# Kernel tuning notes

Hardware: AMD Instinct MI355X
Metric: run time of the kernel (lower is better)

Reference implementation:

```python
import jax, jax.numpy as jnp
import numpy as np

H = 1024

def setup_inputs() -> dict:
    key = jax.random.key(0)
    ks = jax.random.split(key, 9)
    s = 1.0 / np.sqrt(H)
    x = jax.random.normal(ks[0], (4, 2048, H), dtype=jnp.float32)
    Wq = jax.random.uniform(ks[1], (H, H), jnp.float32, -s, s)
    bq = jax.random.uniform(ks[2], (H,), jnp.float32, -s, s)
    Wk = jax.random.uniform(ks[3], (H, H), jnp.float32, -s, s)
    bk = jax.random.uniform(ks[4], (H,), jnp.float32, -s, s)
    Wv = jax.random.uniform(ks[5], (H, H), jnp.float32, -s, s)
    bv = jax.random.uniform(ks[6], (H,), jnp.float32, -s, s)
    Wo = jax.random.uniform(ks[7], (H, H), jnp.float32, -s, s)
    bo = jax.random.uniform(ks[8], (H,), jnp.float32, -s, s)
    return {"x": x, "Wq": Wq, "bq": bq, "Wk": Wk, "bk": bk,
            "Wv": Wv, "bv": bv, "Wo": Wo, "bo": bo}

def reference(x, Wq, bq, Wk, bk, Wv, bv, Wo, bo):
    # Linear uses y = x @ W.T + b (torch convention: W is [out, in])
    q = jnp.einsum('bsd,ed->bse', x, Wq) + bq
    k = jnp.einsum('bsd,ed->bse', x, Wk) + bk
    v = jnp.einsum('bsd,ed->bse', x, Wv) + bv
    scale = q.shape[-1] ** 0.5
    attn = jnp.einsum('bqe,bke->bqk', q, k) / scale  # [B,S,S]
    attn = jax.nn.softmax(attn, axis=-1)
    out = jnp.einsum('bqk,bke->bqe', attn, v)
    return jnp.einsum('bse,oe->bso', out, Wo) + bo
```

## Files before the change

### kernel.cpp

```cpp
#include <hip/hip_runtime.h>

typedef short  short4v __attribute__((ext_vector_type(4)));
typedef short  short8v __attribute__((ext_vector_type(8)));
typedef __bf16 bf16x8  __attribute__((ext_vector_type(8)));
typedef float  f32x4   __attribute__((ext_vector_type(4)));
typedef float  float4v __attribute__((ext_vector_type(4)));

__device__ __forceinline__ short f2bf(float f) {
  unsigned u = __builtin_bit_cast(unsigned, f);
  u += 0x7fffu + ((u >> 16) & 1u);
  return (short)(u >> 16);
}
__device__ __forceinline__ float bf2f(short h) {
  unsigned u = ((unsigned)(unsigned short)h) << 16;
  return __builtin_bit_cast(float, u);
}
__device__ __forceinline__ bf16x8 ld8(const short* p) {
  return __builtin_bit_cast(bf16x8, *reinterpret_cast<const short8v*>(p));
}

__global__ __launch_bounds__(256) void k_cvt(const float* __restrict__ in,
                                             short* __restrict__ out, int n4) {
  int i = blockIdx.x * 256 + threadIdx.x;
  if (i >= n4) return;
  float4v v = *reinterpret_cast<const float4v*>(in + (long)i * 4);
  short4v o;
  o[0] = f2bf(v[0]); o[1] = f2bf(v[1]); o[2] = f2bf(v[2]); o[3] = f2bf(v[3]);
  *reinterpret_cast<short4v*>(out + (long)i * 4) = o;
}

__global__ __launch_bounds__(256) void k_cvtT(const float* __restrict__ i0,
    const float* __restrict__ i1, const float* __restrict__ i2,
    const float* __restrict__ i3, short* __restrict__ o0, short* __restrict__ o1,
    short* __restrict__ o2, short* __restrict__ o3) {
  const int z = blockIdx.z;
  const float* in = z == 0 ? i0 : z == 1 ? i1 : z == 2 ? i2 : i3;
  short* out = z == 0 ? o0 : z == 1 ? o1 : z == 2 ? o2 : o3;
  __shared__ float tile[16][17];
  const int lx = threadIdx.x & 15, ly = threadIdx.x >> 4;
  const int bx = blockIdx.x << 4, by = blockIdx.y << 4;
  float v = in[(long)(by + ly) * 1024 + bx + lx];
  if (z == 3) {
    out[(long)(by + ly) * 1024 + bx + lx] = f2bf(v);
    return;
  }
  tile[ly][lx] = v;
  __syncthreads();
  out[(long)(bx + ly) * 1024 + by + lx] = f2bf(tile[lx][ly]);
}

__global__ __launch_bounds__(256) void k_vecprep(
    const short* __restrict__ wkT, const float* __restrict__ bq,
    const float* __restrict__ Wo, const float* __restrict__ bv,
    float* __restrict__ bvec, float* __restrict__ bvp) {
  const int row = blockIdx.x * 4 + (threadIdx.x >> 6), lane = threadIdx.x & 63;
  float s = 0.f;
  if (blockIdx.z == 0) {
    const short* xr = wkT + (long)row * 1024 + lane * 16;
    short8v a0 = *reinterpret_cast<const short8v*>(xr);
    short8v a1 = *reinterpret_cast<const short8v*>(xr + 8);
#pragma unroll
    for (int j = 0; j < 8; ++j) s += bf2f(a0[j]) * bq[lane * 16 + j];
#pragma unroll
    for (int j = 0; j < 8; ++j) s += bf2f(a1[j]) * bq[lane * 16 + 8 + j];
  } else {
#pragma unroll
    for (int j = 0; j < 16; ++j)
      s += Wo[(long)row * 1024 + j * 64 + lane] * bv[j * 64 + lane];
  }
#pragma unroll
  for (int off = 32; off; off >>= 1) s += __shfl_xor(s, off);
  if (lane == 0) (blockIdx.z == 0 ? bvec : bvp)[row] = s;
}

__global__ __launch_bounds__(256) void k_rowdot(const short* __restrict__ X,
    const float* __restrict__ v, float* __restrict__ o) {
  const int row = blockIdx.x * 4 + (threadIdx.x >> 6), lane = threadIdx.x & 63;
  const short* xr = X + (long)row * 1024 + lane * 16;
  short8v a0 = *reinterpret_cast<const short8v*>(xr);
  short8v a1 = *reinterpret_cast<const short8v*>(xr + 8);
  float s = 0.f;
#pragma unroll
  for (int j = 0; j < 8; ++j) s += bf2f(a0[j]) * v[lane * 16 + j];
#pragma unroll
  for (int j = 0; j < 8; ++j) s += bf2f(a1[j]) * v[lane * 16 + 8 + j];
#pragma unroll
  for (int off = 32; off; off >>= 1) s += __shfl_xor(s, off);
  if (lane == 0) o[row] = s;
}

template <int MODE>
__global__ __launch_bounds__(256, 3) void k_gemm(
    const short* __restrict__ A, const short* __restrict__ B,
    const float* __restrict__ b0p, float* __restrict__ b1p,
    void* __restrict__ C0,
    int K, int lda, int ldb, long sA, long sB, long sC, int ldC) {
  __shared__ __align__(16) short lsA[128 * 64];
  __shared__ __align__(16) short lsB[128 * 64];
  __shared__ float invL[128];
  const int tid = threadIdx.x;
  const int lane = tid & 63, wid = tid >> 6;
  const int wr = wid >> 1, wc = wid & 1;
  const int fr = lane & 15, fq = lane >> 4;
  const int bm = blockIdx.x * 128, bn = blockIdx.y * 128;
  const int bz = blockIdx.z;
  const short* Ab = A + (long)bz * sA;
  const short* Bb = B + (long)bz * sB;

  if constexpr (MODE == 4) {
    if (tid < 128) {
      const float* pr = b1p + ((long)bz * 2048 + bm + tid) * 32;
      float s = 0.f;
#pragma unroll
      for (int j = 0; j < 32; ++j) s += pr[j];
      invL[tid] = 1.0f / s;
    }
  }

  f32x4 acc[4][4] = {};

  for (int kt = 0; kt < K; kt += 64) {
    __syncthreads();
#pragma unroll
    for (int c = 0; c < 4; ++c) {
      const int idx = c * 256 + tid;
      const int row = idx >> 3, colh = (idx & 7) << 3;
      const short* ga = Ab + (long)(bm + row) * lda + kt + colh;
      const short* gb = Bb + (long)(bn + row) * ldb + kt + colh;
      __builtin_amdgcn_global_load_lds(
          (const __attribute__((address_space(1))) void*)ga,
          (__attribute__((address_space(3))) void*)&lsA[idx * 8], 16, 0, 0);
      __builtin_amdgcn_global_load_lds(
          (const __attribute__((address_space(1))) void*)gb,
          (__attribute__((address_space(3))) void*)&lsB[idx * 8], 16, 0, 0);
    }
    __syncthreads();
#pragma unroll
    for (int ks = 0; ks < 64; ks += 32) {
      bf16x8 a[4], b[4];
#pragma unroll
      for (int m = 0; m < 4; ++m)
        a[m] = ld8(&lsA[(wr * 64 + m * 16 + fr) * 64 + ks + fq * 8]);
#pragma unroll
      for (int n = 0; n < 4; ++n)
        b[n] = ld8(&lsB[(wc * 64 + n * 16 + fr) * 64 + ks + fq * 8]);
#pragma unroll
      for (int m = 0; m < 4; ++m)
#pragma unroll
        for (int n = 0; n < 4; ++n)
          acc[m][n] = __builtin_amdgcn_mfma_f32_16x16x32_bf16(a[m], b[n], acc[m][n], 0, 0, 0);
    }
  }

  if constexpr (MODE == 3) {
    constexpr float c = 0.03125f * 1.44269504f;
    short* O = (short*)C0 + (long)bz * sC;
    float wv[4];
#pragma unroll
    for (int n = 0; n < 4; ++n)
      wv[n] = b0p[(long)bz * 2048 + bn + wc * 64 + n * 16 + fr];
#pragma unroll
    for (int m = 0; m < 4; ++m) {
#pragma unroll
      for (int i = 0; i < 4; ++i) {
        const int row = bm + wr * 64 + m * 16 + fq * 4 + i;
        float rs = 0.f;
#pragma unroll
        for (int n = 0; n < 4; ++n) {
          float e = exp2f((acc[m][n][i] + wv[n]) * c);
          O[(long)row * ldC + bn + wc * 64 + n * 16 + fr] = f2bf(e);
          rs += e;
        }
        rs += __shfl_xor(rs, 1); rs += __shfl_xor(rs, 2);
        rs += __shfl_xor(rs, 4); rs += __shfl_xor(rs, 8);
        if (fr == 0)
          b1p[((long)bz * 2048 + row) * 32 + (blockIdx.y << 1) + wc] = rs;
      }
    }
  } else {
#pragma unroll
    for (int n = 0; n < 4; ++n) {
      const int coll = wc * 64 + n * 16 + fr;
#pragma unroll
      for (int m = 0; m < 4; ++m) {
        const int rl0 = wr * 64 + m * 16 + fq * 4;
#pragma unroll
        for (int i = 0; i < 4; ++i) {
          const float vacc = acc[m][n][i];
          const long row = bm + rl0 + i, col = bn + coll;
          if constexpr (MODE == 0) {
            ((short*)C0)[((long)bz * sC) + row * ldC + col] = f2bf(vacc);
          } else if constexpr (MODE == 5) {
            ((short*)C0)[row * ldC + col] = f2bf(vacc + b0p[row]);
          } else {
            float* O = (float*)C0 + (long)bz * sC;
            O[row * ldC + col] = vacc * invL[rl0 + i] + b0p[col];
          }
        }
      }
    }
  }
}

extern "C" void kernel_launch(void* const* d_in, const int* in_sizes, int n_in,
                              void* d_out, int out_size, void* d_ws, size_t ws_size,
                              hipStream_t stream) {
  const float* x  = (const float*)d_in[0];
  const float* Wq = (const float*)d_in[1];
  const float* bq = (const float*)d_in[2];
  const float* Wk = (const float*)d_in[3];
  const float* Wv = (const float*)d_in[5];
  const float* bv = (const float*)d_in[6];
  const float* Wo = (const float*)d_in[7];
  const float* bo = (const float*)d_in[8];

  char* ws = (char*)d_ws;
  short* xb   = (short*)ws; ws += 8192L * 1024 * 2;
  short* wkT  = (short*)ws; ws += 1024L * 1024 * 2;
  short* wob  = (short*)ws; ws += 1024L * 1024 * 2;
  short* wqT  = (short*)ws; ws += 1024L * 1024 * 2;
  short* wvT  = (short*)ws; ws += 1024L * 1024 * 2;
  short* mt   = (short*)ws; ws += 1024L * 1024 * 2;
  short* wv2  = (short*)ws; ws += 1024L * 1024 * 2;
  short* T    = (short*)ws; ws += 8192L * 1024 * 2;
  short* vTp  = (short*)ws; ws += 1024L * 8192 * 2;
  short* Sc   = (short*)ws; ws += 4L * 2048 * 2048 * 2;
  float* psum = (float*)ws; ws += 4L * 2048 * 32 * 4;
  float* w8   = (float*)ws; ws += 8192L * 4;
  float* bvec = (float*)ws; ws += 1024L * 4;
  float* bvp  = (float*)ws; ws += 1024L * 4;

  dim3 b256(256);
  k_cvt<<<8192, b256, 0, stream>>>(x, xb, 2097152);
  k_cvtT<<<dim3(64, 64, 4), b256, 0, stream>>>(
      Wk, Wq, Wv, Wo, wkT, wqT, wvT, wob);
  k_vecprep<<<dim3(256, 1, 2), b256, 0, stream>>>(wkT, bq, Wo, bv, bvec, bvp);
  k_rowdot<<<2048, b256, 0, stream>>>(xb, bvec, w8);

  k_gemm<0><<<dim3(8, 8, 2), b256, 0, stream>>>(
      wkT, wqT, nullptr, nullptr, mt,
      1024, 1024, 1024, 1024L * 1024, 1024L * 1024, 1024L * 1024, 1024);
  k_gemm<0><<<dim3(64, 8, 1), b256, 0, stream>>>(
      xb, mt, nullptr, nullptr, T, 1024, 1024, 1024, 0, 0, 0, 1024);
  k_gemm<5><<<dim3(8, 64, 1), b256, 0, stream>>>(
      wv2, xb, bvp, nullptr, vTp, 1024, 1024, 1024, 0, 0, 0, 8192);
  k_gemm<3><<<dim3(16, 16, 4), b256, 0, stream>>>(
      T, xb, w8, psum, Sc,
      1024, 1024, 1024, 2048L * 1024, 2048L * 1024, 2048L * 2048, 2048);
  k_gemm<4><<<dim3(16, 8, 4), b256, 0, stream>>>(
      Sc, vTp, bo, psum, (float*)d_out,
      2048, 2048, 8192, 2048L * 2048, 2048, 2048L * 1024, 1024);
}
```

Measured before the change: 212.3 us.

## Merge T/V GEMMs and rowdot into one launch; fold softmax scale into weights

```diff
diff --git a/kernel.cpp b/kernel.cpp
--- a/kernel.cpp
+++ b/kernel.cpp
@@ -18,6 +18,8 @@
 __device__ __forceinline__ bf16x8 ld8(const short* p) {
   return __builtin_bit_cast(bf16x8, *reinterpret_cast<const short8v*>(p));
 }
+
+__constant__ const float kExpScale = 0.04508422f;
 
 __global__ __launch_bounds__(256) void k_cvt(const float* __restrict__ in,
                                              short* __restrict__ out, int n4) {
@@ -29,24 +31,48 @@
   *reinterpret_cast<short4v*>(out + (long)i * 4) = o;
 }
 
-__global__ __launch_bounds__(256) void k_cvtT(const float* __restrict__ i0,
+__global__ __launch_bounds__(256) void k_wprep(const float* __restrict__ i0,
     const float* __restrict__ i1, const float* __restrict__ i2,
     const float* __restrict__ i3, short* __restrict__ o0, short* __restrict__ o1,
     short* __restrict__ o2, short* __restrict__ o3) {
   const int z = blockIdx.z;
   const float* in = z == 0 ? i0 : z == 1 ? i1 : z == 2 ? i2 : i3;
   short* out = z == 0 ? o0 : z == 1 ? o1 : z == 2 ? o2 : o3;
-  __shared__ float tile[16][17];
-  const int lx = threadIdx.x & 15, ly = threadIdx.x >> 4;
-  const int bx = blockIdx.x << 4, by = blockIdx.y << 4;
-  float v = in[(long)(by + ly) * 1024 + bx + lx];
+  const float sc = (z == 1) ? kExpScale : 1.0f;
+  const int tid = threadIdx.x;
+  const int c0 = blockIdx.x << 6;
+  const int r0 = blockIdx.y << 7;
   if (z == 3) {
-    out[(long)(by + ly) * 1024 + bx + lx] = f2bf(v);
+#pragma unroll
+    for (int j = 0; j < 8; ++j) {
+      int idx = j * 256 + tid;
+      int r = idx >> 4, c4 = (idx & 15) << 2;
+      float4v v = *reinterpret_cast<const float4v*>(in + (long)(r0 + r) * 1024 + c0 + c4);
+      short4v o;
+      o[0] = f2bf(v[0]); o[1] = f2bf(v[1]); o[2] = f2bf(v[2]); o[3] = f2bf(v[3]);
+      *reinterpret_cast<short4v*>(out + (long)(r0 + r) * 1024 + c0 + c4) = o;
+    }
     return;
   }
-  tile[ly][lx] = v;
+  __shared__ float tile[128][65];
+#pragma unroll
+  for (int j = 0; j < 8; ++j) {
+    int idx = j * 256 + tid;
+    int r = idx >> 4, c4 = (idx & 15) << 2;
+    float4v v = *reinterpret_cast<const float4v*>(in + (long)(r0 + r) * 1024 + c0 + c4);
+    tile[r][c4 + 0] = v[0] * sc; tile[r][c4 + 1] = v[1] * sc;
+    tile[r][c4 + 2] = v[2] * sc; tile[r][c4 + 3] = v[3] * sc;
+  }
   __syncthreads();
-  out[(long)(bx + ly) * 1024 + by + lx] = f2bf(tile[lx][ly]);
+#pragma unroll
+  for (int j = 0; j < 8; ++j) {
+    int idx = j * 256 + tid;
+    int rO = idx >> 5, g4 = (idx & 31) << 2;
+    short4v o;
+    o[0] = f2bf(tile[g4 + 0][rO]); o[1] = f2bf(tile[g4 + 1][rO]);
+    o[2] = f2bf(tile[g4 + 2][rO]); o[3] = f2bf(tile[g4 + 3][rO]);
+    *reinterpret_cast<short4v*>(out + (long)(c0 + rO) * 1024 + r0 + g4) = o;
+  }
 }
 
 __global__ __launch_bounds__(256) void k_vecprep(
@@ -63,6 +89,7 @@
     for (int j = 0; j < 8; ++j) s += bf2f(a0[j]) * bq[lane * 16 + j];
 #pragma unroll
     for (int j = 0; j < 8; ++j) s += bf2f(a1[j]) * bq[lane * 16 + 8 + j];
+    s *= kExpScale;
   } else {
 #pragma unroll
     for (int j = 0; j < 16; ++j)
@@ -73,52 +100,15 @@
   if (lane == 0) (blockIdx.z == 0 ? bvec : bvp)[row] = s;
 }
 
-__global__ __launch_bounds__(256) void k_rowdot(const short* __restrict__ X,
-    const float* __restrict__ v, float* __restrict__ o) {
-  const int row = blockIdx.x * 4 + (threadIdx.x >> 6), lane = threadIdx.x & 63;
-  const short* xr = X + (long)row * 1024 + lane * 16;
-  short8v a0 = *reinterpret_cast<const short8v*>(xr);
-  short8v a1 = *reinterpret_cast<const short8v*>(xr + 8);
-  float s = 0.f;
-#pragma unroll
-  for (int j = 0; j < 8; ++j) s += bf2f(a0[j]) * v[lane * 16 + j];
-#pragma unroll
-  for (int j = 0; j < 8; ++j) s += bf2f(a1[j]) * v[lane * 16 + 8 + j];
-#pragma unroll
-  for (int off = 32; off; off >>= 1) s += __shfl_xor(s, off);
-  if (lane == 0) o[row] = s;
-}
-
-template <int MODE>
-__global__ __launch_bounds__(256, 3) void k_gemm(
-    const short* __restrict__ A, const short* __restrict__ B,
-    const float* __restrict__ b0p, float* __restrict__ b1p,
-    void* __restrict__ C0,
-    int K, int lda, int ldb, long sA, long sB, long sC, int ldC) {
+__device__ __forceinline__ void gemm_loop(const short* __restrict__ Ab,
+    const short* __restrict__ Bb, int K, int lda, int ldb, int bm, int bn,
+    f32x4 (&acc)[4][4]) {
   __shared__ __align__(16) short lsA[128 * 64];
   __shared__ __align__(16) short lsB[128 * 64];
-  __shared__ float invL[128];
   const int tid = threadIdx.x;
   const int lane = tid & 63, wid = tid >> 6;
   const int wr = wid >> 1, wc = wid & 1;
   const int fr = lane & 15, fq = lane >> 4;
-  const int bm = blockIdx.x * 128, bn = blockIdx.y * 128;
-  const int bz = blockIdx.z;
-  const short* Ab = A + (long)bz * sA;
-  const short* Bb = B + (long)bz * sB;
-
-  if constexpr (MODE == 4) {
-    if (tid < 128) {
-      const float* pr = b1p + ((long)bz * 2048 + bm + tid) * 32;
-      float s = 0.f;
-#pragma unroll
-      for (int j = 0; j < 32; ++j) s += pr[j];
-      invL[tid] = 1.0f / s;
-    }
-  }
-
-  f32x4 acc[4][4] = {};
-
   for (int kt = 0; kt < K; kt += 64) {
     __syncthreads();
 #pragma unroll
@@ -151,9 +141,36 @@
           acc[m][n] = __builtin_amdgcn_mfma_f32_16x16x32_bf16(a[m], b[n], acc[m][n], 0, 0, 0);
     }
   }
+}
+
+template <int MODE>
+__global__ __launch_bounds__(256, 3) void k_gemm(
+    const short* __restrict__ A, const short* __restrict__ B,
+    const float* __restrict__ b0p, float* __restrict__ b1p,
+    void* __restrict__ C0,
+    int K, int lda, int ldb, long sA, long sB, long sC, int ldC) {
+  __shared__ float invL[128];
+  const int tid = threadIdx.x;
+  const int lane = tid & 63, wid = tid >> 6;
+  const int wr = wid >> 1, wc = wid & 1;
+  const int fr = lane & 15, fq = lane >> 4;
+  const int bm = blockIdx.x * 128, bn = blockIdx.y * 128;
+  const int bz = blockIdx.z;
+
+  if constexpr (MODE == 4) {
+    if (tid < 128) {
+      const float* pr = b1p + ((long)bz * 2048 + bm + tid) * 32;
+      float s = 0.f;
+#pragma unroll
+      for (int j = 0; j < 32; ++j) s += pr[j];
+      invL[tid] = 1.0f / s;
+    }
+  }
+
+  f32x4 acc[4][4] = {};
+  gemm_loop(A + (long)bz * sA, B + (long)bz * sB, K, lda, ldb, bm, bn, acc);
 
   if constexpr (MODE == 3) {
-    constexpr float c = 0.03125f * 1.44269504f;
     short* O = (short*)C0 + (long)bz * sC;
     float wv[4];
 #pragma unroll
@@ -167,7 +184,7 @@
         float rs = 0.f;
 #pragma unroll
         for (int n = 0; n < 4; ++n) {
-          float e = exp2f((acc[m][n][i] + wv[n]) * c);
+          float e = exp2f(acc[m][n][i] + wv[n]);
           O[(long)row * ldC + bn + wc * 64 + n * 16 + fr] = f2bf(e);
           rs += e;
         }
@@ -190,13 +207,64 @@
           const long row = bm + rl0 + i, col = bn + coll;
           if constexpr (MODE == 0) {
             ((short*)C0)[((long)bz * sC) + row * ldC + col] = f2bf(vacc);
-          } else if constexpr (MODE == 5) {
-            ((short*)C0)[row * ldC + col] = f2bf(vacc + b0p[row]);
           } else {
             float* O = (float*)C0 + (long)bz * sC;
             O[row * ldC + col] = vacc * invL[rl0 + i] + b0p[col];
           }
         }
+      }
+    }
+  }
+}
+
+__global__ __launch_bounds__(256, 3) void k_gemmTV(
+    const short* __restrict__ xb, const short* __restrict__ mt,
+    const short* __restrict__ wv2, const float* __restrict__ bvp,
+    const float* __restrict__ bvec, short* __restrict__ T,
+    short* __restrict__ vTp, float* __restrict__ w8) {
+  const int tid = threadIdx.x;
+  const int lane = tid & 63, wid = tid >> 6;
+  if (blockIdx.z == 2) {
+    const int rbase = (blockIdx.x * 8 + blockIdx.y) * 16;
+#pragma unroll
+    for (int rr = 0; rr < 4; ++rr) {
+      const int row = rbase + wid * 4 + rr;
+      const short* xr = xb + (long)row * 1024 + lane * 16;
+      short8v a0 = *reinterpret_cast<const short8v*>(xr);
+      short8v a1 = *reinterpret_cast<const short8v*>(xr + 8);
+      float s = 0.f;
+#pragma unroll
+      for (int j = 0; j < 8; ++j) s += bf2f(a0[j]) * bvec[lane * 16 + j];
+#pragma unroll
+      for (int j = 0; j < 8; ++j) s += bf2f(a1[j]) * bvec[lane * 16 + 8 + j];
+#pragma unroll
+      for (int off = 32; off; off >>= 1) s += __shfl_xor(s, off);
+      if (lane == 0) w8[row] = s;
+    }
+    return;
+  }
+  const short *A, *B; const float* bias; short* C; int ldC, bm, bn;
+  if (blockIdx.z == 0) {
+    A = xb; B = mt; bias = nullptr; C = T; ldC = 1024;
+    bm = blockIdx.x * 128; bn = blockIdx.y * 128;
+  } else {
+    A = wv2; B = xb; bias = bvp; C = vTp; ldC = 8192;
+    bm = blockIdx.y * 128; bn = blockIdx.x * 128;
+  }
+  f32x4 acc[4][4] = {};
+  gemm_loop(A, B, 1024, 1024, 1024, bm, bn, acc);
+  const int wr = wid >> 1, wc = wid & 1;
+  const int fr = lane & 15, fq = lane >> 4;
+#pragma unroll
+  for (int n = 0; n < 4; ++n) {
+    const int col = bn + wc * 64 + n * 16 + fr;
+#pragma unroll
+    for (int m = 0; m < 4; ++m) {
+      const int row0 = bm + wr * 64 + m * 16 + fq * 4;
+#pragma unroll
+      for (int i = 0; i < 4; ++i) {
+        const float bvr = bias ? bias[row0 + i] : 0.f;
+        C[(long)(row0 + i) * ldC + col] = f2bf(acc[m][n][i] + bvr);
       }
     }
   }
@@ -232,18 +300,15 @@
 
   dim3 b256(256);
   k_cvt<<<8192, b256, 0, stream>>>(x, xb, 2097152);
-  k_cvtT<<<dim3(64, 64, 4), b256, 0, stream>>>(
+  k_wprep<<<dim3(16, 8, 4), b256, 0, stream>>>(
       Wk, Wq, Wv, Wo, wkT, wqT, wvT, wob);
   k_vecprep<<<dim3(256, 1, 2), b256, 0, stream>>>(wkT, bq, Wo, bv, bvec, bvp);
-  k_rowdot<<<2048, b256, 0, stream>>>(xb, bvec, w8);
 
   k_gemm<0><<<dim3(8, 8, 2), b256, 0, stream>>>(
       wkT, wqT, nullptr, nullptr, mt,
       1024, 1024, 1024, 1024L * 1024, 1024L * 1024, 1024L * 1024, 1024);
-  k_gemm<0><<<dim3(64, 8, 1), b256, 0, stream>>>(
-      xb, mt, nullptr, nullptr, T, 1024, 1024, 1024, 0, 0, 0, 1024);
-  k_gemm<5><<<dim3(8, 64, 1), b256, 0, stream>>>(
-      wv2, xb, bvp, nullptr, vTp, 1024, 1024, 1024, 0, 0, 0, 8192);
+  k_gemmTV<<<dim3(64, 8, 3), b256, 0, stream>>>(
+      xb, mt, wv2, bvp, bvec, T, vTp, w8);
   k_gemm<3><<<dim3(16, 16, 4), b256, 0, stream>>>(
       T, xb, w8, psum, Sc,
       1024, 1024, 1024, 2048L * 1024, 2048L * 1024, 2048L * 2048, 2048);
```

Result: faster. 200.8 us (-5.4%).
